# Kernel optimization log

Hardware: AMD Instinct MI355X
Metric: run time of the kernel (lower is better)

The kernel has to match this reference:

```python
import jax, jax.numpy as jnp
import numpy as np

EPS = 1e-08


def setup_inputs() -> dict:
    key = jax.random.key(0)
    k1, k2 = jax.random.split(key)
    B, K, H = 8, 8000, 512
    inputs = jax.random.normal(k1, (B, K, H), dtype=jnp.float32)
    gamma = jax.random.normal(k2, (1, H), dtype=jnp.float32) * 0.05  # 'random_normal' init
    beta = jnp.zeros((1, H), dtype=jnp.float32)
    return {"inputs": inputs, "gamma": gamma, "beta": beta}


def reference(inputs, gamma, beta):
    # Cumulative (causal) layer norm: at step k, normalize frame k using
    # mean/var computed over the prefix inputs[:, :k+1, :] (time and feature dims).
    B, K, H = inputs.shape
    # Running sums over time of per-frame sums across features -> O(K) scan.
    step_sum = jnp.sum(inputs, axis=-1)          # [B, K]
    step_sumsq = jnp.sum(inputs * inputs, axis=-1)  # [B, K]
    cum_sum = jnp.cumsum(step_sum, axis=1)       # [B, K]
    cum_sumsq = jnp.cumsum(step_sumsq, axis=1)   # [B, K]
    count = (jnp.arange(1, K + 1, dtype=inputs.dtype) * H)  # [K] elements in each prefix
    mean = cum_sum / count                        # [B, K]
    var = cum_sumsq / count - mean * mean         # [B, K]
    inv_std = 1.0 / jnp.sqrt(var + EPS)           # matches (var + eps) ** 0.5
    # gamma/beta: (1, H) broadcast over [B, K, H]
    out = gamma * ((inputs - mean[..., None]) * inv_std[..., None]) + beta
    return out
```

## Files before the change

kernel.cpp:

```cpp
#include <hip/hip_runtime.h>
#include <math.h>


#define HDIM 512
#define F4H (HDIM / 4)
#define SEG 64
#define BATCHES 8

typedef float f32x4 __attribute__((ext_vector_type(4)));

__global__ __launch_bounds__(256) void k_seg_sums(
    const float* __restrict__ in, float* __restrict__ ssum,
    float* __restrict__ ssq, double* __restrict__ segS,
    double* __restrict__ segQ, int K, int segsPerBatch)
{
    const int lane = threadIdx.x & 63;
    const int wid  = threadIdx.x >> 6;
    const int segGlobal = blockIdx.x;
    const int b   = segGlobal / segsPerBatch;
    const int seg = segGlobal % segsPerBatch;
    const int k0  = seg * SEG;

    double accS = 0.0, accQ = 0.0;
    #pragma unroll 4
    for (int i = 0; i < SEG / 4; ++i) {
        const int fk = k0 + wid * (SEG / 4) + i;
        if (fk < K) {
            const float4* p = (const float4*)in + ((size_t)b * K + fk) * F4H;
            float4 a = p[lane];
            float4 c = p[lane + 64];
            float s = (a.x + a.y) + (a.z + a.w) + (c.x + c.y) + (c.z + c.w);
            float q = (a.x * a.x + a.y * a.y) + (a.z * a.z + a.w * a.w)
                    + (c.x * c.x + c.y * c.y) + (c.z * c.z + c.w * c.w);
            #pragma unroll
            for (int off = 32; off >= 1; off >>= 1) {
                s += __shfl_xor(s, off);
                q += __shfl_xor(q, off);
            }
            if (lane == 0) {
                ssum[(size_t)b * K + fk] = s;
                ssq[(size_t)b * K + fk]  = q;
            }
            accS += (double)s;
            accQ += (double)q;
        }
    }
    __shared__ double wS[4], wQ[4];
    if (lane == 0) { wS[wid] = accS; wQ[wid] = accQ; }
    __syncthreads();
    if (threadIdx.x == 0) {
        segS[segGlobal] = wS[0] + wS[1] + wS[2] + wS[3];
        segQ[segGlobal] = wQ[0] + wQ[1] + wQ[2] + wQ[3];
    }
}

__global__ __launch_bounds__(512) void k_seg_scan(
    const double* __restrict__ segS, const double* __restrict__ segQ,
    double* __restrict__ offS, double* __restrict__ offQ, int segsPerBatch)
{
    const int lane = threadIdx.x & 63;
    const int b = threadIdx.x >> 6;
    if (b >= BATCHES) return;

    double carryS = 0.0, carryQ = 0.0;
    for (int base = 0; base < segsPerBatch; base += 64) {
        const int sidx = base + lane;
        const bool v = sidx < segsPerBatch;
        double s = v ? segS[(size_t)b * segsPerBatch + sidx] : 0.0;
        double q = v ? segQ[(size_t)b * segsPerBatch + sidx] : 0.0;
        const double sIn = s, qIn = q;
        #pragma unroll
        for (int off = 1; off < 64; off <<= 1) {
            double s2 = __shfl_up(s, off);
            double q2 = __shfl_up(q, off);
            if (lane >= off) { s += s2; q += q2; }
        }
        if (v) {
            offS[(size_t)b * segsPerBatch + sidx] = carryS + s - sIn;
            offQ[(size_t)b * segsPerBatch + sidx] = carryQ + q - qIn;
        }
        carryS += __shfl(s, 63);
        carryQ += __shfl(q, 63);
    }
}

__global__ __launch_bounds__(256) void k_frame_stats(
    const float* __restrict__ ssum, const float* __restrict__ ssq,
    const double* __restrict__ offS, const double* __restrict__ offQ,
    float* __restrict__ mean, float* __restrict__ istd,
    int K, int segsPerBatch)
{
    const int lane = threadIdx.x & 63;
    const int segGlobal = blockIdx.x * 4 + (threadIdx.x >> 6);
    if (segGlobal >= BATCHES * segsPerBatch) return;
    const int b   = segGlobal / segsPerBatch;
    const int seg = segGlobal % segsPerBatch;
    const int k   = seg * SEG + lane;

    double s = 0.0, q = 0.0;
    if (k < K) {
        s = (double)ssum[(size_t)b * K + k];
        q = (double)ssq[(size_t)b * K + k];
    }
    #pragma unroll
    for (int off = 1; off < 64; off <<= 1) {
        double s2 = __shfl_up(s, off);
        double q2 = __shfl_up(q, off);
        if (lane >= off) { s += s2; q += q2; }
    }
    if (k < K) {
        s += offS[segGlobal];
        q += offQ[segGlobal];
        const double cnt = (double)(k + 1) * (double)HDIM;
        const double m = s / cnt;
        const double var = q / cnt - m * m;
        mean[(size_t)b * K + k] = (float)m;
        istd[(size_t)b * K + k] = (float)(1.0 / sqrt(var + 1e-8));
    }
}

__global__ __launch_bounds__(256) void k_normalize(
    const float* __restrict__ in, const float* __restrict__ gamma,
    const float* __restrict__ beta, const float* __restrict__ mean,
    const float* __restrict__ istd, float* __restrict__ out, int nframes)
{
    const int t = threadIdx.x;
    const int frame = blockIdx.x * 2 + (t >> 7);
    const int c = t & (F4H - 1);
    if (frame >= nframes) return;

    const float m = mean[frame];
    const float r = istd[frame];
    const float4 g  = ((const float4*)gamma)[c];
    const float4 be = ((const float4*)beta)[c];
    const float4 x  = ((const float4*)in)[(size_t)frame * F4H + c];

    f32x4 o;
    o.x = g.x * ((x.x - m) * r) + be.x;
    o.y = g.y * ((x.y - m) * r) + be.y;
    o.z = g.z * ((x.z - m) * r) + be.z;
    o.w = g.w * ((x.w - m) * r) + be.w;
    __builtin_nontemporal_store(o, (f32x4*)out + (size_t)frame * F4H + c);
}

extern "C" void kernel_launch(void* const* d_in, const int* in_sizes, int n_in,
                              void* d_out, int out_size, void* d_ws, size_t ws_size,
                              hipStream_t stream)
{
    const float* in    = (const float*)d_in[0];
    const float* gamma = (const float*)d_in[1];
    const float* beta  = (const float*)d_in[2];
    float* out = (float*)d_out;

    const int H = in_sizes[1];
    const int BK = in_sizes[0] / H;
    const int B = BATCHES;
    const int K = BK / B;
    const int segsPerBatch = (K + SEG - 1) / SEG;
    const int NSEG = B * segsPerBatch;
    (void)H; (void)n_in; (void)out_size; (void)ws_size;

    float* ssum = (float*)d_ws;
    float* ssq  = ssum + BK;
    float* mean = ssq + BK;
    float* istd = mean + BK;
    double* segS = (double*)(istd + BK);
    double* segQ = segS + NSEG;
    double* offS = segQ + NSEG;
    double* offQ = offS + NSEG;

    k_seg_sums<<<dim3(NSEG), dim3(256), 0, stream>>>(
        in, ssum, ssq, segS, segQ, K, segsPerBatch);
    k_seg_scan<<<dim3(1), dim3(512), 0, stream>>>(
        segS, segQ, offS, offQ, segsPerBatch);
    k_frame_stats<<<dim3((NSEG + 3) / 4), dim3(256), 0, stream>>>(
        ssum, ssq, offS, offQ, mean, istd, K, segsPerBatch);
    k_normalize<<<dim3((BK + 1) / 2), dim3(256), 0, stream>>>(
        in, gamma, beta, mean, istd, out, BK);
}
```

Before: 68.55 us.

## Fuse cumulative layer norm into single cooperative kernel with on-chip frame caching

Replaces the four-kernel pipeline (segment sums, segment scan, frame stats, normalize) with one cooperative kernel. Each block reduces 64 frames, publishes its segment sums, does a grid-wide sync, then computes its prefix offset by summing earlier segments and normalizes. Part of each block's input is kept in LDS and registers so the second pass rereads less from global memory. This removes three launches and the global round-trips for per-frame stats, at the cost of a grid barrier, full co-residency of 1000 blocks, and a redundant O(segments) prefix sum per block.

```diff
diff --git a/kernel.cpp b/kernel.cpp
--- a/kernel.cpp
+++ b/kernel.cpp
@@ -1,13 +1,149 @@
 #include <hip/hip_runtime.h>
+#include <hip/hip_cooperative_groups.h>
 #include <math.h>
+
+namespace cg = cooperative_groups;
 
 
 #define HDIM 512
 #define F4H (HDIM / 4)
+#define BATCHES 8
+#define KLEN 8000
+#define FPB 64
+#define SEGS (KLEN / FPB)
+#define NBLK (BATCHES * SEGS)
 #define SEG 64
-#define BATCHES 8
 
 typedef float f32x4 __attribute__((ext_vector_type(4)));
+typedef unsigned long long u64;
+
+__global__ __launch_bounds__(256, 4) void cln_coop(
+    const float* __restrict__ in, const float* __restrict__ gamma,
+    const float* __restrict__ beta, float* __restrict__ out,
+    double* __restrict__ segS, double* __restrict__ segQ)
+{
+    __shared__ float4 xs[16][F4H];
+    __shared__ float4 gb4[256];
+    __shared__ float fsum[FPB], fsq[FPB], meanS[FPB], istdS[FPB];
+    __shared__ double wS[4], wQ[4];
+
+    const int tid  = threadIdx.x;
+    const int lane = tid & 63;
+    const int wid  = tid >> 6;
+    const int bx   = blockIdx.x;
+    const int b    = bx / SEGS;
+    const int s    = bx % SEGS;
+
+    if (tid < 128) gb4[tid] = ((const float4*)gamma)[tid];
+    else           gb4[tid] = ((const float4*)beta)[tid - 128];
+
+    const size_t rowBase = ((size_t)b * KLEN + (size_t)s * FPB + wid * 16) * F4H;
+    const float4* p = (const float4*)in + rowBase;
+
+    float4 rA[6], rB[6];
+    double accS = 0.0, accQ = 0.0;
+    #pragma unroll
+    for (int fi = 0; fi < 16; ++fi) {
+        float4 a = p[(size_t)fi * F4H + lane];
+        float4 c = p[(size_t)fi * F4H + 64 + lane];
+        float sv = (a.x + a.y) + (a.z + a.w) + (c.x + c.y) + (c.z + c.w);
+        float qv = (a.x * a.x + a.y * a.y) + (a.z * a.z + a.w * a.w)
+                 + (c.x * c.x + c.y * c.y) + (c.z * c.z + c.w * c.w);
+        #pragma unroll
+        for (int off = 32; off >= 1; off >>= 1) {
+            sv += __shfl_xor(sv, off);
+            qv += __shfl_xor(qv, off);
+        }
+        if (lane == 0) { fsum[wid * 16 + fi] = sv; fsq[wid * 16 + fi] = qv; }
+        accS += (double)sv;
+        accQ += (double)qv;
+        if (fi < 4)       { xs[wid * 4 + fi][lane] = a; xs[wid * 4 + fi][64 + lane] = c; }
+        else if (fi < 10) { rA[fi - 4] = a; rB[fi - 4] = c; }
+    }
+    if (lane == 0) { wS[wid] = accS; wQ[wid] = accQ; }
+    __syncthreads();
+    if (tid == 0) {
+        double S = wS[0] + wS[1] + wS[2] + wS[3];
+        double Q = wQ[0] + wQ[1] + wQ[2] + wQ[3];
+        __hip_atomic_store((u64*)&segS[bx], __double_as_longlong(S),
+                           __ATOMIC_RELEASE, __HIP_MEMORY_SCOPE_AGENT);
+        __hip_atomic_store((u64*)&segQ[bx], __double_as_longlong(Q),
+                           __ATOMIC_RELEASE, __HIP_MEMORY_SCOPE_AGENT);
+    }
+
+    cg::this_grid().sync();
+
+    if (wid == 0) {
+        double es = 0.0, eq = 0.0;
+        for (int base = 0; base < s; base += 64) {
+            const int j = base + lane;
+            double a = 0.0, q2 = 0.0;
+            if (j < s) {
+                a  = __longlong_as_double(__hip_atomic_load((u64*)&segS[b * SEGS + j],
+                        __ATOMIC_ACQUIRE, __HIP_MEMORY_SCOPE_AGENT));
+                q2 = __longlong_as_double(__hip_atomic_load((u64*)&segQ[b * SEGS + j],
+                        __ATOMIC_ACQUIRE, __HIP_MEMORY_SCOPE_AGENT));
+            }
+            es += a; eq += q2;
+        }
+        #pragma unroll
+        for (int off = 32; off >= 1; off >>= 1) {
+            es += __shfl_xor(es, off);
+            eq += __shfl_xor(eq, off);
+        }
+        double sc = (double)fsum[lane], qc = (double)fsq[lane];
+        #pragma unroll
+        for (int off = 1; off < 64; off <<= 1) {
+            double s2 = __shfl_up(sc, off);
+            double q2 = __shfl_up(qc, off);
+            if (lane >= off) { sc += s2; qc += q2; }
+        }
+        sc += es; qc += eq;
+        const double cnt = (double)(s * FPB + lane + 1) * (double)HDIM;
+        const double m   = sc / cnt;
+        const double var = qc / cnt - m * m;
+        meanS[lane] = (float)m;
+        istdS[lane] = (float)(1.0 / sqrt(var + 1e-8));
+    }
+    __syncthreads();
+
+    const float4 g0  = gb4[lane],       g1  = gb4[64 + lane];
+    const float4 be0 = gb4[128 + lane], be1 = gb4[192 + lane];
+    f32x4* o4 = (f32x4*)out + rowBase;
+
+#define APPLY(fi, a, c) {                                                   \
+        const float m = meanS[wid * 16 + (fi)];                             \
+        const float r = istdS[wid * 16 + (fi)];                             \
+        f32x4 o0, o1;                                                       \
+        o0.x = g0.x * ((a.x - m) * r) + be0.x;                              \
+        o0.y = g0.y * ((a.y - m) * r) + be0.y;                              \
+        o0.z = g0.z * ((a.z - m) * r) + be0.z;                              \
+        o0.w = g0.w * ((a.w - m) * r) + be0.w;                              \
+        o1.x = g1.x * ((c.x - m) * r) + be1.x;                              \
+        o1.y = g1.y * ((c.y - m) * r) + be1.y;                              \
+        o1.z = g1.z * ((c.z - m) * r) + be1.z;                              \
+        o1.w = g1.w * ((c.w - m) * r) + be1.w;                              \
+        __builtin_nontemporal_store(o0, o4 + (size_t)(fi) * F4H + lane);    \
+        __builtin_nontemporal_store(o1, o4 + (size_t)(fi) * F4H + 64 + lane); }
+
+    #pragma unroll
+    for (int fi = 10; fi < 16; ++fi) {
+        float4 a = p[(size_t)fi * F4H + lane];
+        float4 c = p[(size_t)fi * F4H + 64 + lane];
+        APPLY(fi, a, c);
+    }
+    #pragma unroll
+    for (int fi = 4; fi < 10; ++fi) {
+        APPLY(fi, rA[fi - 4], rB[fi - 4]);
+    }
+    #pragma unroll
+    for (int fi = 0; fi < 4; ++fi) {
+        float4 a = xs[wid * 4 + fi][lane];
+        float4 c = xs[wid * 4 + fi][64 + lane];
+        APPLY(fi, a, c);
+    }
+#undef APPLY
+}
 
 __global__ __launch_bounds__(256) void k_seg_sums(
     const float* __restrict__ in, float* __restrict__ ssum,
@@ -152,29 +288,48 @@
     const float* beta  = (const float*)d_in[2];
     float* out = (float*)d_out;
 
-    const int H = in_sizes[1];
+    const int H  = in_sizes[1];
     const int BK = in_sizes[0] / H;
-    const int B = BATCHES;
-    const int K = BK / B;
-    const int segsPerBatch = (K + SEG - 1) / SEG;
-    const int NSEG = B * segsPerBatch;
-    (void)H; (void)n_in; (void)out_size; (void)ws_size;
-
-    float* ssum = (float*)d_ws;
+    const int K  = BK / BATCHES;
+    (void)n_in; (void)out_size; (void)ws_size;
+
+    double* segS = (double*)d_ws;
+    double* segQ = segS + NBLK;
+    float* ssum = (float*)(segQ + NBLK);
     float* ssq  = ssum + BK;
     float* mean = ssq + BK;
     float* istd = mean + BK;
-    double* segS = (double*)(istd + BK);
-    double* segQ = segS + NSEG;
-    double* offS = segQ + NSEG;
-    double* offQ = offS + NSEG;
-
-    k_seg_sums<<<dim3(NSEG), dim3(256), 0, stream>>>(
-        in, ssum, ssq, segS, segQ, K, segsPerBatch);
-    k_seg_scan<<<dim3(1), dim3(512), 0, stream>>>(
-        segS, segQ, offS, offQ, segsPerBatch);
-    k_frame_stats<<<dim3((NSEG + 3) / 4), dim3(256), 0, stream>>>(
-        ssum, ssq, offS, offQ, mean, istd, K, segsPerBatch);
-    k_normalize<<<dim3((BK + 1) / 2), dim3(256), 0, stream>>>(
-        in, gamma, beta, mean, istd, out, BK);
-}
+    double* fsegS = (double*)(istd + BK);
+    double* fsegQ = fsegS + BATCHES * ((K + SEG - 1) / SEG);
+    double* offS  = fsegQ + BATCHES * ((K + SEG - 1) / SEG);
+    double* offQ  = offS  + BATCHES * ((K + SEG - 1) / SEG);
+
+    bool coop = (H == HDIM) && (K == KLEN) && (in_sizes[0] == BATCHES * KLEN * HDIM);
+    if (coop) {
+        int dev = 0, nb = 0, cus = 0;
+        if (hipGetDevice(&dev) != hipSuccess) coop = false;
+        if (coop && hipOccupancyMaxActiveBlocksPerMultiprocessor(
+                        &nb, (const void*)cln_coop, 256, 0) != hipSuccess) coop = false;
+        if (coop && hipDeviceGetAttribute(&cus, hipDeviceAttributeMultiprocessorCount,
+                                          dev) != hipSuccess) coop = false;
+        if (coop && (long)nb * cus < NBLK) coop = false;
+    }
+
+    if (coop) {
+        void* args[] = {(void*)&in, (void*)&gamma, (void*)&beta,
+                        (void*)&out, (void*)&segS, (void*)&segQ};
+        hipLaunchCooperativeKernel((const void*)cln_coop, dim3(NBLK), dim3(256),
+                                   args, 0, stream);
+    } else {
+        const int segsPerBatch = (K + SEG - 1) / SEG;
+        const int NSEG = BATCHES * segsPerBatch;
+        k_seg_sums<<<dim3(NSEG), dim3(256), 0, stream>>>(
+            in, ssum, ssq, fsegS, fsegQ, K, segsPerBatch);
+        k_seg_scan<<<dim3(1), dim3(512), 0, stream>>>(
+            fsegS, fsegQ, offS, offQ, segsPerBatch);
+        k_frame_stats<<<dim3((NSEG + 3) / 4), dim3(256), 0, stream>>>(
+            ssum, ssq, offS, offQ, mean, istd, K, segsPerBatch);
+        k_normalize<<<dim3((BK + 1) / 2), dim3(256), 0, stream>>>(
+            in, gamma, beta, mean, istd, out, BK);
+    }
+}
```

Result: no change. 69.09 us (+0.8%).

## Fuse segment scan, frame stats and normalize into one kernel

Applied to the files above, without the earlier changes.

Replaces the single-block segment scan, the per-frame stats kernel and the normalize kernel with one kernel per segment. Wave 0 of each block recomputes its exclusive prefix by summing all earlier segment totals, then scans the frame sums and writes mean/istd to shared memory for the other waves to use while normalizing. This removes two kernel launches, a serial single-block scan, and the global round-trip of mean/istd. In exchange every block redundantly reads up to ~125 prior segment totals, giving O(segs^2) total reads, though these are small and cached.

```diff
diff --git a/kernel.cpp b/kernel.cpp
--- a/kernel.cpp
+++ b/kernel.cpp
@@ -54,93 +54,89 @@
     }
 }
 
-__global__ __launch_bounds__(512) void k_seg_scan(
-    const double* __restrict__ segS, const double* __restrict__ segQ,
-    double* __restrict__ offS, double* __restrict__ offQ, int segsPerBatch)
+__global__ __launch_bounds__(256) void k_norm_fused(
+    const float* __restrict__ in, const float* __restrict__ gamma,
+    const float* __restrict__ beta, const float* __restrict__ ssum,
+    const float* __restrict__ ssq, const double* __restrict__ segS,
+    const double* __restrict__ segQ, float* __restrict__ out,
+    int K, int segsPerBatch)
 {
-    const int lane = threadIdx.x & 63;
-    const int b = threadIdx.x >> 6;
-    if (b >= BATCHES) return;
+    __shared__ float meanS[SEG], istdS[SEG];
 
-    double carryS = 0.0, carryQ = 0.0;
-    for (int base = 0; base < segsPerBatch; base += 64) {
-        const int sidx = base + lane;
-        const bool v = sidx < segsPerBatch;
-        double s = v ? segS[(size_t)b * segsPerBatch + sidx] : 0.0;
-        double q = v ? segQ[(size_t)b * segsPerBatch + sidx] : 0.0;
-        const double sIn = s, qIn = q;
+    const int tid  = threadIdx.x;
+    const int lane = tid & 63;
+    const int wid  = tid >> 6;
+    const int segGlobal = blockIdx.x;
+    const int b = segGlobal / segsPerBatch;
+    const int s = segGlobal % segsPerBatch;
+    const int k0 = s * SEG;
+
+    const f32x4 g0  = ((const f32x4*)gamma)[lane];
+    const f32x4 g1  = ((const f32x4*)gamma)[lane + 64];
+    const f32x4 be0 = ((const f32x4*)beta)[lane];
+    const f32x4 be1 = ((const f32x4*)beta)[lane + 64];
+
+    if (wid == 0) {
+        double es = 0.0, eq = 0.0;
+        for (int base = 0; base < s; base += 64) {
+            const int j = base + lane;
+            if (j < s) {
+                es += segS[(size_t)b * segsPerBatch + j];
+                eq += segQ[(size_t)b * segsPerBatch + j];
+            }
+        }
+        #pragma unroll
+        for (int off = 32; off >= 1; off >>= 1) {
+            es += __shfl_xor(es, off);
+            eq += __shfl_xor(eq, off);
+        }
+        const int k = k0 + lane;
+        double sc = 0.0, qc = 0.0;
+        if (k < K) {
+            sc = (double)ssum[(size_t)b * K + k];
+            qc = (double)ssq[(size_t)b * K + k];
+        }
         #pragma unroll
         for (int off = 1; off < 64; off <<= 1) {
-            double s2 = __shfl_up(s, off);
-            double q2 = __shfl_up(q, off);
-            if (lane >= off) { s += s2; q += q2; }
+            double s2 = __shfl_up(sc, off);
+            double q2 = __shfl_up(qc, off);
+            if (lane >= off) { sc += s2; qc += q2; }
         }
-        if (v) {
-            offS[(size_t)b * segsPerBatch + sidx] = carryS + s - sIn;
-            offQ[(size_t)b * segsPerBatch + sidx] = carryQ + q - qIn;
+        sc += es; qc += eq;
+        if (k < K) {
+            const double cnt = (double)(k + 1) * (double)HDIM;
+            const double m   = sc / cnt;
+            const double var = qc / cnt - m * m;
+            meanS[lane] = (float)m;
+            istdS[lane] = (float)(1.0 / sqrt(var + 1e-8));
         }
-        carryS += __shfl(s, 63);
-        carryQ += __shfl(q, 63);
     }
-}
+    __syncthreads();
 
-__global__ __launch_bounds__(256) void k_frame_stats(
-    const float* __restrict__ ssum, const float* __restrict__ ssq,
-    const double* __restrict__ offS, const double* __restrict__ offQ,
-    float* __restrict__ mean, float* __restrict__ istd,
-    int K, int segsPerBatch)
-{
-    const int lane = threadIdx.x & 63;
-    const int segGlobal = blockIdx.x * 4 + (threadIdx.x >> 6);
-    if (segGlobal >= BATCHES * segsPerBatch) return;
-    const int b   = segGlobal / segsPerBatch;
-    const int seg = segGlobal % segsPerBatch;
-    const int k   = seg * SEG + lane;
-
-    double s = 0.0, q = 0.0;
-    if (k < K) {
-        s = (double)ssum[(size_t)b * K + k];
-        q = (double)ssq[(size_t)b * K + k];
+    #pragma unroll 4
+    for (int i = 0; i < SEG / 4; ++i) {
+        const int fi = wid * (SEG / 4) + i;
+        const int k = k0 + fi;
+        if (k < K) {
+            const f32x4* p = (const f32x4*)in + ((size_t)b * K + k) * F4H;
+            const f32x4 a = p[lane];
+            const f32x4 c = p[lane + 64];
+            const float m = meanS[fi];
+            const float r = istdS[fi];
+            f32x4 o0, o1;
+            o0.x = g0.x * ((a.x - m) * r) + be0.x;
+            o0.y = g0.y * ((a.y - m) * r) + be0.y;
+            o0.z = g0.z * ((a.z - m) * r) + be0.z;
+            o0.w = g0.w * ((a.w - m) * r) + be0.w;
+            o1.x = g1.x * ((c.x - m) * r) + be1.x;
+            o1.y = g1.y * ((c.y - m) * r) + be1.y;
+            o1.z = g1.z * ((c.z - m) * r) + be1.z;
+            o1.w = g1.w * ((c.w - m) * r) + be1.w;
+            f32x4* q = (f32x4*)out + ((size_t)b * K + k) * F4H;
+            __builtin_nontemporal_store(o0, q + lane);
+            __builtin_nontemporal_store(o1, q + lane + 64);
+        }
     }
-    #pragma unroll
-    for (int off = 1; off < 64; off <<= 1) {
-        double s2 = __shfl_up(s, off);
-        double q2 = __shfl_up(q, off);
-        if (lane >= off) { s += s2; q += q2; }
-    }
-    if (k < K) {
-        s += offS[segGlobal];
-        q += offQ[segGlobal];
-        const double cnt = (double)(k + 1) * (double)HDIM;
-        const double m = s / cnt;
-        const double var = q / cnt - m * m;
-        mean[(size_t)b * K + k] = (float)m;
-        istd[(size_t)b * K + k] = (float)(1.0 / sqrt(var + 1e-8));
-    }
-}
-
-__global__ __launch_bounds__(256) void k_normalize(
-    const float* __restrict__ in, const float* __restrict__ gamma,
-    const float* __restrict__ beta, const float* __restrict__ mean,
-    const float* __restrict__ istd, float* __restrict__ out, int nframes)
-{
-    const int t = threadIdx.x;
-    const int frame = blockIdx.x * 2 + (t >> 7);
-    const int c = t & (F4H - 1);
-    if (frame >= nframes) return;
-
-    const float m = mean[frame];
-    const float r = istd[frame];
-    const float4 g  = ((const float4*)gamma)[c];
-    const float4 be = ((const float4*)beta)[c];
-    const float4 x  = ((const float4*)in)[(size_t)frame * F4H + c];
-
-    f32x4 o;
-    o.x = g.x * ((x.x - m) * r) + be.x;
-    o.y = g.y * ((x.y - m) * r) + be.y;
-    o.z = g.z * ((x.z - m) * r) + be.z;
-    o.w = g.w * ((x.w - m) * r) + be.w;
-    __builtin_nontemporal_store(o, (f32x4*)out + (size_t)frame * F4H + c);
 }
 
 extern "C" void kernel_launch(void* const* d_in, const int* in_sizes, int n_in,
@@ -154,27 +150,18 @@
 
     const int H = in_sizes[1];
     const int BK = in_sizes[0] / H;
-    const int B = BATCHES;
-    const int K = BK / B;
+    const int K = BK / BATCHES;
     const int segsPerBatch = (K + SEG - 1) / SEG;
-    const int NSEG = B * segsPerBatch;
+    const int NSEG = BATCHES * segsPerBatch;
     (void)H; (void)n_in; (void)out_size; (void)ws_size;
 
     float* ssum = (float*)d_ws;
     float* ssq  = ssum + BK;
-    float* mean = ssq + BK;
-    float* istd = mean + BK;
-    double* segS = (double*)(istd + BK);
+    double* segS = (double*)(ssq + BK);
     double* segQ = segS + NSEG;
-    double* offS = segQ + NSEG;
-    double* offQ = offS + NSEG;
 
     k_seg_sums<<<dim3(NSEG), dim3(256), 0, stream>>>(
         in, ssum, ssq, segS, segQ, K, segsPerBatch);
-    k_seg_scan<<<dim3(1), dim3(512), 0, stream>>>(
-        segS, segQ, offS, offQ, segsPerBatch);
-    k_frame_stats<<<dim3((NSEG + 3) / 4), dim3(256), 0, stream>>>(
-        ssum, ssq, offS, offQ, mean, istd, K, segsPerBatch);
-    k_normalize<<<dim3((BK + 1) / 2), dim3(256), 0, stream>>>(
-        in, gamma, beta, mean, istd, out, BK);
+    k_norm_fused<<<dim3(NSEG), dim3(256), 0, stream>>>(
+        in, gamma, beta, ssum, ssq, segS, segQ, out, K, segsPerBatch);
 }
```

After: 67.13 us. 2.1% less time.
